# Optimization experiments

Hardware: AMD Instinct MI355X
Metric: run time of the kernel (lower is better)

The kernel has to match this reference:

```python
import jax, jax.numpy as jnp
import numpy as np

B, NH, T, D = 2, 16, 2048, 64

def setup_inputs() -> dict:
    key = jax.random.key(0)
    kq, kk, kv = jax.random.split(key, 3)
    Q = jax.random.normal(kq, (B, NH, T, D), dtype=jnp.float32)
    K = jax.random.normal(kk, (B, NH, T, D), dtype=jnp.float32)
    V = jax.random.normal(kv, (B, NH, T, D), dtype=jnp.float32)
    return {"Q": Q, "K": K, "V": V}

def reference(Q, K, V):
    # scores: [B, nh, T, T]
    Dh = Q.shape[-1]
    scale = 1.0 / jnp.sqrt(jnp.asarray(Dh, Q.dtype))
    scores = jnp.einsum('bhtd,bhsd->bhts', Q, K) * scale
    Tq = Q.shape[2]
    causal = jnp.tril(jnp.ones((Tq, Tq), dtype=bool))
    scores = jnp.where(causal, scores, jnp.asarray(-jnp.inf, scores.dtype))
    attn = jax.nn.softmax(scores, axis=-1)
    return jnp.einsum('bhts,bhsd->bhtd', attn, V)
```

## Files before the change

### kernel.cpp

```cpp
#include <hip/hip_runtime.h>
#include <hip/hip_bf16.h>


typedef __bf16 bf16;
typedef __bf16 bf16x2 __attribute__((ext_vector_type(2)));
typedef __bf16 bf16x4 __attribute__((ext_vector_type(4)));
typedef __bf16 bf16x8 __attribute__((ext_vector_type(8)));
typedef float floatx4 __attribute__((ext_vector_type(4)));

#define T_SEQ 2048
#define DH 64
#define TKS 32
#define BHN 32
#define CEXP 0.18033688011112042f

__device__ __forceinline__ void gload16(const bf16* g, bf16* l) {
    __builtin_amdgcn_global_load_lds(
        (const __attribute__((address_space(1))) void*)g,
        (__attribute__((address_space(3))) void*)l, 16, 0, 0);
}

__global__ __launch_bounds__(256) void prep(const float* __restrict__ K,
                                            const float* __restrict__ V,
                                            bf16* __restrict__ Kb,
                                            bf16* __restrict__ Vt) {
    const int bid = (int)blockIdx.x;
    const int tid = (int)threadIdx.x;
    if (bid < 512) {
        size_t i = ((size_t)bid * 256 + tid) * 8;
        #pragma unroll
        for (int it = 0; it < 4; ++it) {
            float4 a = *(const float4*)(K + i + 0);
            float4 b = *(const float4*)(K + i + 4);
            bf16x8 o;
            o[0]=(bf16)(a.x*CEXP); o[1]=(bf16)(a.y*CEXP); o[2]=(bf16)(a.z*CEXP); o[3]=(bf16)(a.w*CEXP);
            o[4]=(bf16)(b.x*CEXP); o[5]=(bf16)(b.y*CEXP); o[6]=(bf16)(b.z*CEXP); o[7]=(bf16)(b.w*CEXP);
            *(bf16x8*)(Kb + i) = o;
            i += (size_t)512 * 256 * 8;
        }
        return;
    }
    __shared__ bf16 tile[2][64][72];
    const int vb = bid - 512;
    const int bh = vb & (BHN - 1);
    const int tp = (vb >> 5) * 128;
    #pragma unroll
    for (int tt = 0; tt < 2; ++tt) {
        const int r = tid >> 2;
        const int c = (tid & 3) * 16;
        const float* s = V + ((size_t)bh * T_SEQ + tp + tt * 64 + r) * DH + c;
        float4 f0 = *(const float4*)(s + 0);
        float4 f1 = *(const float4*)(s + 4);
        float4 f2 = *(const float4*)(s + 8);
        float4 f3 = *(const float4*)(s + 12);
        bf16x8 p0, p1;
        p0[0]=(bf16)f0.x; p0[1]=(bf16)f0.y; p0[2]=(bf16)f0.z; p0[3]=(bf16)f0.w;
        p0[4]=(bf16)f1.x; p0[5]=(bf16)f1.y; p0[6]=(bf16)f1.z; p0[7]=(bf16)f1.w;
        p1[0]=(bf16)f2.x; p1[1]=(bf16)f2.y; p1[2]=(bf16)f2.z; p1[3]=(bf16)f2.w;
        p1[4]=(bf16)f3.x; p1[5]=(bf16)f3.y; p1[6]=(bf16)f3.z; p1[7]=(bf16)f3.w;
        *(bf16x8*)&tile[tt][r][c + 0] = p0;
        *(bf16x8*)&tile[tt][r][c + 8] = p1;
    }
    __syncthreads();
    #pragma unroll
    for (int tt = 0; tt < 2; ++tt) {
        const int d   = tid >> 2;
        const int tch = (tid & 3) * 16;
        bf16x8 o0, o1;
        #pragma unroll
        for (int j = 0; j < 8; ++j) { o0[j] = tile[tt][tch + j][d]; o1[j] = tile[tt][tch + 8 + j][d]; }
        bf16* o = Vt + ((size_t)bh * DH + d) * T_SEQ + tp + tt * 64 + tch;
        *(bf16x8*)(o + 0) = o0;
        *(bf16x8*)(o + 8) = o1;
    }
}

__global__ __launch_bounds__(256, 2)
void fa_fwd(const float* __restrict__ Qg, const bf16* __restrict__ Kb,
            const bf16* __restrict__ Vt, float* __restrict__ Og)
{
    __shared__ __align__(16) bf16 smem[24576];

    const int gid = (int)blockIdx.x;
    const int bh  = gid & (BHN - 1);
    const int m   = gid >> 5;
    const int B   = 64 - 2 * m;
    const int qh  = (31 - m) * 64;
    const int ql  = m * 64;

    const int tid  = (int)threadIdx.x;
    const int wave = tid >> 6;
    const int lane = tid & 63;
    const int quad = lane >> 4;
    const int l16  = lane & 15;
    const int psw  = (l16 >> 1) & 3;

    const int tw0 = (wave < 2) ? wave * 17 : 34 + (wave - 2) * 16;
    const int tw1 = tw0 + ((wave < 2) ? 17 : 16);

    bf16* W = smem + wave * 6144;

    const bf16* Kbh = Kb + (size_t)bh * (T_SEQ * DH);
    const bf16* Vbh = Vt + (size_t)bh * (DH * T_SEQ);
    const size_t qrb = (size_t)bh * T_SEQ;

    const int rl  = lane >> 3;
    const int kch = (lane & 7) ^ (rl & 7);
    const int vr  = lane >> 2;
    const int vch = (lane & 3) ^ ((lane >> 3) & 3);

    bool heavyNow = (tw0 < B);
    int  qbase    = heavyNow ? qh : ql;
    bool hasPark  = false;

    bf16x8 qb[4][2];
    auto loadQ = [&](int qb0) {
        #pragma unroll
        for (int nt = 0; nt < 4; ++nt) {
            const int qrow = qb0 + nt * 16 + l16;
            #pragma unroll
            for (int kk = 0; kk < 2; ++kk) {
                const float* s = Qg + (qrb + qrow) * DH + kk * 32 + quad * 8;
                float4 f0 = *(const float4*)(s);
                float4 f1 = *(const float4*)(s + 4);
                bf16x8 t;
                t[0]=(bf16)f0.x; t[1]=(bf16)f0.y; t[2]=(bf16)f0.z; t[3]=(bf16)f0.w;
                t[4]=(bf16)f1.x; t[5]=(bf16)f1.y; t[6]=(bf16)f1.z; t[7]=(bf16)f1.w;
                qb[nt][kk] = t;
            }
        }
    };
    loadQ(qbase);

    floatx4 oacc[4][4];
    #pragma unroll
    for (int mt = 0; mt < 4; ++mt)
        #pragma unroll
        for (int nt = 0; nt < 4; ++nt) oacc[mt][nt] = (floatx4){0.f,0.f,0.f,0.f};
    float lpart[4] = {0.f, 0.f, 0.f, 0.f};
    bf16x4 parked[16];
    #pragma unroll
    for (int f = 0; f < 16; ++f) parked[f] = (bf16x4){(bf16)0.f,(bf16)0.f,(bf16)0.f,(bf16)0.f};
    float lpark[4] = {0.f, 0.f, 0.f, 0.f};

    auto kTileOf = [&](int t) { return (t < B) ? t : (t - B); };

    auto stageK = [&](int kt, bf16* dst) {
        const bf16* kg = Kbh + (size_t)kt * TKS * DH;
        #pragma unroll
        for (int g = 0; g < 4; ++g)
            gload16(kg + (size_t)(g * 8 + rl) * DH + kch * 8, dst + g * 512);
    };
    auto stageV = [&](int kt, bf16* dst) {
        const bf16* vg = Vbh + kt * TKS;
        #pragma unroll
        for (int g = 0; g < 4; ++g)
            gload16(vg + (size_t)(g * 16 + vr) * T_SEQ + vch * 8, dst + g * 512);
    };

    auto pk2 = [&](float a, float b) -> unsigned {
        bf16x2 h; h[0] = (bf16)a; h[1] = (bf16)b;
        return __builtin_bit_cast(unsigned, h);
    };

    stageK(kTileOf(tw0), W);
    stageV(kTileOf(tw0), W + 4096);

    for (int t = tw0; t < tw1; ++t) {
        if (heavyNow && t == B) {
            #pragma unroll
            for (int f = 0; f < 16; ++f) {
                bf16x4 w;
                #pragma unroll
                for (int e = 0; e < 4; ++e) w[e] = (bf16)oacc[f >> 2][f & 3][e];
                parked[f] = w;
            }
            #pragma unroll
            for (int nt = 0; nt < 4; ++nt) { lpark[nt] = lpart[nt]; lpart[nt] = 0.f; }
            #pragma unroll
            for (int mt = 0; mt < 4; ++mt)
                #pragma unroll
                for (int nt = 0; nt < 4; ++nt) oacc[mt][nt] = (floatx4){0.f,0.f,0.f,0.f};
            hasPark = true;
            heavyNow = false;
            qbase = ql;
            loadQ(ql);
        }

        const int cur = (t - tw0) & 1;
        bf16* Kcur = W + cur * 2048;
        bf16* Vcur = W + 4096;
        const int kt = kTileOf(t);
        const int k0 = kt * TKS;

        const bool pf = (t + 1 < tw1);
        if (pf) {
            stageK(kTileOf(t + 1), W + (cur ^ 1) * 2048);
            __builtin_amdgcn_s_waitcnt(0x0F78);
        } else {
            __builtin_amdgcn_s_waitcnt(0x0F70);
        }

        floatx4 sa[2][4];
        #pragma unroll
        for (int mt = 0; mt < 2; ++mt)
            #pragma unroll
            for (int nt = 0; nt < 4; ++nt) sa[mt][nt] = (floatx4){0.f,0.f,0.f,0.f};
        __builtin_amdgcn_s_setprio(1);
        #pragma unroll
        for (int kk = 0; kk < 2; ++kk) {
            #pragma unroll
            for (int mt = 0; mt < 2; ++mt) {
                bf16x8 kf = *(const bf16x8*)&Kcur[(mt * 16 + l16) * 64 + (((kk * 4 + quad) ^ (l16 & 7)) * 8)];
                #pragma unroll
                for (int nt = 0; nt < 4; ++nt)
                    sa[mt][nt] = __builtin_amdgcn_mfma_f32_16x16x32_bf16(kf, qb[nt][kk], sa[mt][nt], 0, 0, 0);
            }
        }
        __builtin_amdgcn_s_setprio(0);
        if (k0 + TKS - 1 > qbase) {
            #pragma unroll
            for (int mt = 0; mt < 2; ++mt)
                #pragma unroll
                for (int nt = 0; nt < 4; ++nt) {
                    const int qg = qbase + nt * 16 + l16;
                    #pragma unroll
                    for (int r = 0; r < 4; ++r) {
                        const int keyg = k0 + mt * 16 + quad * 4 + r;
                        if (keyg > qg) sa[mt][nt][r] = -INFINITY;
                    }
                }
        }
        bf16x8 pfr[4];
        #pragma unroll
        for (int nt = 0; nt < 4; ++nt) {
            float p0[4], p1[4];
            #pragma unroll
            for (int r = 0; r < 4; ++r) {
                p0[r] = __builtin_amdgcn_exp2f(sa[0][nt][r]);
                p1[r] = __builtin_amdgcn_exp2f(sa[1][nt][r]);
                lpart[nt] += p0[r] + p1[r];
            }
            unsigned X0 = pk2(p0[0], p0[1]);
            unsigned X1 = pk2(p0[2], p0[3]);
            unsigned Y0 = pk2(p1[0], p1[1]);
            unsigned Y1 = pk2(p1[2], p1[3]);
            asm("v_permlane32_swap_b32 %0, %1" : "+v"(X0), "+v"(Y0));
            asm("v_permlane16_swap_b32 %0, %1" : "+v"(X0), "+v"(Y0));
            asm("v_permlane32_swap_b32 %0, %1" : "+v"(X1), "+v"(Y1));
            asm("v_permlane16_swap_b32 %0, %1" : "+v"(X1), "+v"(Y1));
            uint4 u; u.x = X0; u.y = X1; u.z = Y0; u.w = Y1;
            pfr[nt] = __builtin_bit_cast(bf16x8, u);
        }
        if (pf) __builtin_amdgcn_s_waitcnt(0x0F74);
        bf16x8 vf[4];
        #pragma unroll
        for (int mt = 0; mt < 4; ++mt)
            vf[mt] = *(const bf16x8*)&Vcur[(mt * 16 + l16) * 32 + ((quad ^ psw) * 8)];
        if (pf) {
            __builtin_amdgcn_s_waitcnt(0xC07F);
            stageV(kTileOf(t + 1), Vcur);
        }
        __builtin_amdgcn_s_setprio(1);
        #pragma unroll
        for (int mt = 0; mt < 4; ++mt) {
            #pragma unroll
            for (int nt = 0; nt < 4; ++nt)
                oacc[mt][nt] = __builtin_amdgcn_mfma_f32_16x16x32_bf16(vf[mt], pfr[nt], oacc[mt][nt], 0, 0, 0);
        }
        __builtin_amdgcn_s_setprio(0);
    }

    __syncthreads();
    const bool hH = (tw0 < B);
    const bool hL = (tw1 > B);
    if (wave >= 1 && hH) {
        bf16* a = smem + (wave - 1) * 4608;
        float* al = (float*)(a + 4096);
        #pragma unroll
        for (int f = 0; f < 16; ++f) {
            bf16x4 w;
            if (hasPark) w = parked[f];
            else {
                #pragma unroll
                for (int e = 0; e < 4; ++e) w[e] = (bf16)oacc[f >> 2][f & 3][e];
            }
            *(bf16x4*)&a[(f * 64 + lane) * 4] = w;
        }
        #pragma unroll
        for (int nt = 0; nt < 4; ++nt)
            al[nt * 64 + lane] = hasPark ? lpark[nt] : lpart[nt];
    }
    if (wave >= 2 && hL) {
        bf16* a = smem + (wave + 1) * 4608;
        float* al = (float*)(a + 4096);
        #pragma unroll
        for (int f = 0; f < 16; ++f) {
            bf16x4 w;
            #pragma unroll
            for (int e = 0; e < 4; ++e) w[e] = (bf16)oacc[f >> 2][f & 3][e];
            *(bf16x4*)&a[(f * 64 + lane) * 4] = w;
        }
        #pragma unroll
        for (int nt = 0; nt < 4; ++nt)
            al[nt * 64 + lane] = lpart[nt];
    }
    __syncthreads();

    if (wave <= 1) {
        int qfin;
        if (wave == 0) {
            qfin = qh;
            const int nA = (B > 50) ? 3 : ((B > 34) ? 2 : 1);
            for (int i = 0; i < nA; ++i) {
                const bf16* a = smem + i * 4608;
                const float* al = (const float*)(a + 4096);
                #pragma unroll
                for (int f = 0; f < 16; ++f) {
                    bf16x4 w = *(const bf16x4*)&a[(f * 64 + lane) * 4];
                    #pragma unroll
                    for (int e = 0; e < 4; ++e) oacc[f >> 2][f & 3][e] += (float)w[e];
                }
                #pragma unroll
                for (int nt = 0; nt < 4; ++nt) lpart[nt] += al[nt * 64 + lane];
            }
        } else {
            qfin = ql;
            #pragma unroll
            for (int mt = 0; mt < 4; ++mt)
                #pragma unroll
                for (int nt = 0; nt < 4; ++nt) oacc[mt][nt] = (floatx4){0.f,0.f,0.f,0.f};
            #pragma unroll
            for (int nt = 0; nt < 4; ++nt) lpart[nt] = 0.f;
            const int i0 = (B < 50) ? 3 : 4;
            for (int i = i0; i <= 4; ++i) {
                const bf16* a = smem + i * 4608;
                const float* al = (const float*)(a + 4096);
                #pragma unroll
                for (int f = 0; f < 16; ++f) {
                    bf16x4 w = *(const bf16x4*)&a[(f * 64 + lane) * 4];
                    #pragma unroll
                    for (int e = 0; e < 4; ++e) oacc[f >> 2][f & 3][e] += (float)w[e];
                }
                #pragma unroll
                for (int nt = 0; nt < 4; ++nt) lpart[nt] += al[nt * 64 + lane];
            }
        }
        float invl[4];
        #pragma unroll
        for (int nt = 0; nt < 4; ++nt) {
            float v = lpart[nt];
            v += __shfl_xor(v, 16);
            v += __shfl_xor(v, 32);
            invl[nt] = 1.0f / v;
        }
        #pragma unroll
        for (int nt = 0; nt < 4; ++nt) {
            const size_t qrow = qrb + qfin + nt * 16 + l16;
            #pragma unroll
            for (int mt = 0; mt < 4; ++mt) {
                float4 o;
                o.x = oacc[mt][nt][0] * invl[nt];
                o.y = oacc[mt][nt][1] * invl[nt];
                o.z = oacc[mt][nt][2] * invl[nt];
                o.w = oacc[mt][nt][3] * invl[nt];
                *(float4*)&Og[qrow * DH + mt * 16 + quad * 4] = o;
            }
        }
    }
}

extern "C" void kernel_launch(void* const* d_in, const int* in_sizes, int n_in,
                              void* d_out, int out_size, void* d_ws, size_t ws_size,
                              hipStream_t stream) {
    const float* Q = (const float*)d_in[0];
    const float* K = (const float*)d_in[1];
    const float* V = (const float*)d_in[2];
    float* O = (float*)d_out;
    (void)in_sizes; (void)n_in; (void)out_size; (void)ws_size;

    const size_t nelem = (size_t)BHN * T_SEQ * DH;
    bf16* Kbf = (bf16*)d_ws;
    bf16* Vtb = Kbf + nelem;

    prep<<<dim3(1024), dim3(256), 0, stream>>>(K, V, Kbf, Vtb);
    fa_fwd<<<dim3(512), dim3(256), 0, stream>>>(Q, Kbf, Vtb, O);
}
```

Measured before the change: 120.0 us.

## Replace paired heavy/light query-block balancing with one query block per workgroup

Drops the scheme that paired a heavy and a light 64-row query block in each workgroup (with parked partial accumulators). Each workgroup now handles one query block, and its causal key tiles are split evenly across the four waves. The grid doubles to 1024 blocks, and launch bounds rise to three blocks per CU to improve occupancy and simplify control flow. In exchange, per-block work becomes uneven, so the heavy-first ordering matters for tail balance. The final reduction now splits output rows between two waves.

```diff
diff --git a/kernel.cpp b/kernel.cpp
--- a/kernel.cpp
+++ b/kernel.cpp
@@ -75,18 +75,17 @@
     }
 }
 
-__global__ __launch_bounds__(256, 2)
+__global__ __launch_bounds__(256, 3)
 void fa_fwd(const float* __restrict__ Qg, const bf16* __restrict__ Kb,
             const bf16* __restrict__ Vt, float* __restrict__ Og)
 {
     __shared__ __align__(16) bf16 smem[24576];
 
-    const int gid = (int)blockIdx.x;
-    const int bh  = gid & (BHN - 1);
-    const int m   = gid >> 5;
-    const int B   = 64 - 2 * m;
-    const int qh  = (31 - m) * 64;
-    const int ql  = m * 64;
+    const int gid   = (int)blockIdx.x;
+    const int jt    = 31 - (gid >> 5);
+    const int bh    = gid & (BHN - 1);
+    const int qbase = jt * 64;
+    const int ntile = 2 * jt + 2;
 
     const int tid  = (int)threadIdx.x;
     const int wave = tid >> 6;
@@ -95,8 +94,11 @@
     const int l16  = lane & 15;
     const int psw  = (l16 >> 1) & 3;
 
-    const int tw0 = (wave < 2) ? wave * 17 : 34 + (wave - 2) * 16;
-    const int tw1 = tw0 + ((wave < 2) ? 17 : 16);
+    const int base = ntile >> 2;
+    const int rem  = ntile & 3;
+    const int tw0  = wave * base + ((wave < rem) ? wave : rem);
+    const int cnt  = base + ((wave < rem) ? 1 : 0);
+    const int tw1  = tw0 + cnt;
 
     bf16* W = smem + wave * 6144;
 
@@ -109,15 +111,36 @@
     const int vr  = lane >> 2;
     const int vch = (lane & 3) ^ ((lane >> 3) & 3);
 
-    bool heavyNow = (tw0 < B);
-    int  qbase    = heavyNow ? qh : ql;
-    bool hasPark  = false;
-
-    bf16x8 qb[4][2];
-    auto loadQ = [&](int qb0) {
+    floatx4 oacc[4][4];
+    #pragma unroll
+    for (int mt = 0; mt < 4; ++mt)
+        #pragma unroll
+        for (int nt = 0; nt < 4; ++nt) oacc[mt][nt] = (floatx4){0.f,0.f,0.f,0.f};
+    float lpart[4] = {0.f, 0.f, 0.f, 0.f};
+
+    auto stageK = [&](int kt, bf16* dst) {
+        const bf16* kg = Kbh + (size_t)kt * TKS * DH;
+        #pragma unroll
+        for (int g = 0; g < 4; ++g)
+            gload16(kg + (size_t)(g * 8 + rl) * DH + kch * 8, dst + g * 512);
+    };
+    auto stageV = [&](int kt, bf16* dst) {
+        const bf16* vg = Vbh + kt * TKS;
+        #pragma unroll
+        for (int g = 0; g < 4; ++g)
+            gload16(vg + (size_t)(g * 16 + vr) * T_SEQ + vch * 8, dst + g * 512);
+    };
+
+    auto pk2 = [&](float a, float b) -> unsigned {
+        bf16x2 h; h[0] = (bf16)a; h[1] = (bf16)b;
+        return __builtin_bit_cast(unsigned, h);
+    };
+
+    if (cnt > 0) {
+        bf16x8 qb[4][2];
         #pragma unroll
         for (int nt = 0; nt < 4; ++nt) {
-            const int qrow = qb0 + nt * 16 + l16;
+            const int qrow = qbase + nt * 16 + l16;
             #pragma unroll
             for (int kk = 0; kk < 2; ++kk) {
                 const float* s = Qg + (qrb + qrow) * DH + kk * 32 + quad * 8;
@@ -129,174 +152,102 @@
                 qb[nt][kk] = t;
             }
         }
-    };
-    loadQ(qbase);
-
-    floatx4 oacc[4][4];
-    #pragma unroll
-    for (int mt = 0; mt < 4; ++mt)
-        #pragma unroll
-        for (int nt = 0; nt < 4; ++nt) oacc[mt][nt] = (floatx4){0.f,0.f,0.f,0.f};
-    float lpart[4] = {0.f, 0.f, 0.f, 0.f};
-    bf16x4 parked[16];
-    #pragma unroll
-    for (int f = 0; f < 16; ++f) parked[f] = (bf16x4){(bf16)0.f,(bf16)0.f,(bf16)0.f,(bf16)0.f};
-    float lpark[4] = {0.f, 0.f, 0.f, 0.f};
-
-    auto kTileOf = [&](int t) { return (t < B) ? t : (t - B); };
-
-    auto stageK = [&](int kt, bf16* dst) {
-        const bf16* kg = Kbh + (size_t)kt * TKS * DH;
-        #pragma unroll
-        for (int g = 0; g < 4; ++g)
-            gload16(kg + (size_t)(g * 8 + rl) * DH + kch * 8, dst + g * 512);
-    };
-    auto stageV = [&](int kt, bf16* dst) {
-        const bf16* vg = Vbh + kt * TKS;
-        #pragma unroll
-        for (int g = 0; g < 4; ++g)
-            gload16(vg + (size_t)(g * 16 + vr) * T_SEQ + vch * 8, dst + g * 512);
-    };
-
-    auto pk2 = [&](float a, float b) -> unsigned {
-        bf16x2 h; h[0] = (bf16)a; h[1] = (bf16)b;
-        return __builtin_bit_cast(unsigned, h);
-    };
-
-    stageK(kTileOf(tw0), W);
-    stageV(kTileOf(tw0), W + 4096);
-
-    for (int t = tw0; t < tw1; ++t) {
-        if (heavyNow && t == B) {
-            #pragma unroll
-            for (int f = 0; f < 16; ++f) {
-                bf16x4 w;
-                #pragma unroll
-                for (int e = 0; e < 4; ++e) w[e] = (bf16)oacc[f >> 2][f & 3][e];
-                parked[f] = w;
-            }
-            #pragma unroll
-            for (int nt = 0; nt < 4; ++nt) { lpark[nt] = lpart[nt]; lpart[nt] = 0.f; }
+
+        stageK(tw0, W);
+        stageV(tw0, W + 4096);
+
+        for (int t = tw0; t < tw1; ++t) {
+            const int cur = (t - tw0) & 1;
+            bf16* Kcur = W + cur * 2048;
+            bf16* Vcur = W + 4096;
+            const int k0 = t * TKS;
+
+            const bool pf = (t + 1 < tw1);
+            if (pf) {
+                stageK(t + 1, W + (cur ^ 1) * 2048);
+                __builtin_amdgcn_s_waitcnt(0x0F78);
+            } else {
+                __builtin_amdgcn_s_waitcnt(0x0F70);
+            }
+
+            floatx4 sa[2][4];
+            #pragma unroll
+            for (int mt = 0; mt < 2; ++mt)
+                #pragma unroll
+                for (int nt = 0; nt < 4; ++nt) sa[mt][nt] = (floatx4){0.f,0.f,0.f,0.f};
+            __builtin_amdgcn_s_setprio(1);
+            #pragma unroll
+            for (int kk = 0; kk < 2; ++kk) {
+                #pragma unroll
+                for (int mt = 0; mt < 2; ++mt) {
+                    bf16x8 kf = *(const bf16x8*)&Kcur[(mt * 16 + l16) * 64 + (((kk * 4 + quad) ^ (l16 & 7)) * 8)];
+                    #pragma unroll
+                    for (int nt = 0; nt < 4; ++nt)
+                        sa[mt][nt] = __builtin_amdgcn_mfma_f32_16x16x32_bf16(kf, qb[nt][kk], sa[mt][nt], 0, 0, 0);
+                }
+            }
+            __builtin_amdgcn_s_setprio(0);
+            if (k0 + TKS - 1 > qbase) {
+                #pragma unroll
+                for (int mt = 0; mt < 2; ++mt)
+                    #pragma unroll
+                    for (int nt = 0; nt < 4; ++nt) {
+                        const int qg = qbase + nt * 16 + l16;
+                        #pragma unroll
+                        for (int r = 0; r < 4; ++r) {
+                            const int keyg = k0 + mt * 16 + quad * 4 + r;
+                            if (keyg > qg) sa[mt][nt][r] = -INFINITY;
+                        }
+                    }
+            }
+            bf16x8 pfr[4];
+            #pragma unroll
+            for (int nt = 0; nt < 4; ++nt) {
+                float p0[4], p1[4];
+                #pragma unroll
+                for (int r = 0; r < 4; ++r) {
+                    p0[r] = __builtin_amdgcn_exp2f(sa[0][nt][r]);
+                    p1[r] = __builtin_amdgcn_exp2f(sa[1][nt][r]);
+                    lpart[nt] += p0[r] + p1[r];
+                }
+                unsigned X0 = pk2(p0[0], p0[1]);
+                unsigned X1 = pk2(p0[2], p0[3]);
+                unsigned Y0 = pk2(p1[0], p1[1]);
+                unsigned Y1 = pk2(p1[2], p1[3]);
+                asm("v_permlane32_swap_b32 %0, %1" : "+v"(X0), "+v"(Y0));
+                asm("v_permlane16_swap_b32 %0, %1" : "+v"(X0), "+v"(Y0));
+                asm("v_permlane32_swap_b32 %0, %1" : "+v"(X1), "+v"(Y1));
+                asm("v_permlane16_swap_b32 %0, %1" : "+v"(X1), "+v"(Y1));
+                uint4 u; u.x = X0; u.y = X1; u.z = Y0; u.w = Y1;
+                pfr[nt] = __builtin_bit_cast(bf16x8, u);
+            }
+            if (pf) __builtin_amdgcn_s_waitcnt(0x0F74);
+            bf16x8 vf[4];
             #pragma unroll
             for (int mt = 0; mt < 4; ++mt)
-                #pragma unroll
-                for (int nt = 0; nt < 4; ++nt) oacc[mt][nt] = (floatx4){0.f,0.f,0.f,0.f};
-            hasPark = true;
-            heavyNow = false;
-            qbase = ql;
-            loadQ(ql);
-        }
-
-        const int cur = (t - tw0) & 1;
-        bf16* Kcur = W + cur * 2048;
-        bf16* Vcur = W + 4096;
-        const int kt = kTileOf(t);
-        const int k0 = kt * TKS;
-
-        const bool pf = (t + 1 < tw1);
-        if (pf) {
-            stageK(kTileOf(t + 1), W + (cur ^ 1) * 2048);
-            __builtin_amdgcn_s_waitcnt(0x0F78);
-        } else {
-            __builtin_amdgcn_s_waitcnt(0x0F70);
-        }
-
-        floatx4 sa[2][4];
-        #pragma unroll
-        for (int mt = 0; mt < 2; ++mt)
-            #pragma unroll
-            for (int nt = 0; nt < 4; ++nt) sa[mt][nt] = (floatx4){0.f,0.f,0.f,0.f};
-        __builtin_amdgcn_s_setprio(1);
-        #pragma unroll
-        for (int kk = 0; kk < 2; ++kk) {
-            #pragma unroll
-            for (int mt = 0; mt < 2; ++mt) {
-                bf16x8 kf = *(const bf16x8*)&Kcur[(mt * 16 + l16) * 64 + (((kk * 4 + quad) ^ (l16 & 7)) * 8)];
+                vf[mt] = *(const bf16x8*)&Vcur[(mt * 16 + l16) * 32 + ((quad ^ psw) * 8)];
+            if (pf) {
+                __builtin_amdgcn_s_waitcnt(0xC07F);
+                stageV(t + 1, Vcur);
+            }
+            __builtin_amdgcn_s_setprio(1);
+            #pragma unroll
+            for (int mt = 0; mt < 4; ++mt) {
                 #pragma unroll
                 for (int nt = 0; nt < 4; ++nt)
-                    sa[mt][nt] = __builtin_amdgcn_mfma_f32_16x16x32_bf16(kf, qb[nt][kk], sa[mt][nt], 0, 0, 0);
-            }
-        }
-        __builtin_amdgcn_s_setprio(0);
-        if (k0 + TKS - 1 > qbase) {
-            #pragma unroll
-            for (int mt = 0; mt < 2; ++mt)
-                #pragma unroll
-                for (int nt = 0; nt < 4; ++nt) {
-                    const int qg = qbase + nt * 16 + l16;
-                    #pragma unroll
-                    for (int r = 0; r < 4; ++r) {
-                        const int keyg = k0 + mt * 16 + quad * 4 + r;
-                        if (keyg > qg) sa[mt][nt][r] = -INFINITY;
-                    }
-                }
-        }
-        bf16x8 pfr[4];
-        #pragma unroll
-        for (int nt = 0; nt < 4; ++nt) {
-            float p0[4], p1[4];
-            #pragma unroll
-            for (int r = 0; r < 4; ++r) {
-                p0[r] = __builtin_amdgcn_exp2f(sa[0][nt][r]);
-                p1[r] = __builtin_amdgcn_exp2f(sa[1][nt][r]);
-                lpart[nt] += p0[r] + p1[r];
-            }
-            unsigned X0 = pk2(p0[0], p0[1]);
-            unsigned X1 = pk2(p0[2], p0[3]);
-            unsigned Y0 = pk2(p1[0], p1[1]);
-            unsigned Y1 = pk2(p1[2], p1[3]);
-            asm("v_permlane32_swap_b32 %0, %1" : "+v"(X0), "+v"(Y0));
-            asm("v_permlane16_swap_b32 %0, %1" : "+v"(X0), "+v"(Y0));
-            asm("v_permlane32_swap_b32 %0, %1" : "+v"(X1), "+v"(Y1));
-            asm("v_permlane16_swap_b32 %0, %1" : "+v"(X1), "+v"(Y1));
-            uint4 u; u.x = X0; u.y = X1; u.z = Y0; u.w = Y1;
-            pfr[nt] = __builtin_bit_cast(bf16x8, u);
-        }
-        if (pf) __builtin_amdgcn_s_waitcnt(0x0F74);
-        bf16x8 vf[4];
-        #pragma unroll
-        for (int mt = 0; mt < 4; ++mt)
-            vf[mt] = *(const bf16x8*)&Vcur[(mt * 16 + l16) * 32 + ((quad ^ psw) * 8)];
-        if (pf) {
-            __builtin_amdgcn_s_waitcnt(0xC07F);
-            stageV(kTileOf(t + 1), Vcur);
-        }
-        __builtin_amdgcn_s_setprio(1);
-        #pragma unroll
-        for (int mt = 0; mt < 4; ++mt) {
-            #pragma unroll
-            for (int nt = 0; nt < 4; ++nt)
-                oacc[mt][nt] = __builtin_amdgcn_mfma_f32_16x16x32_bf16(vf[mt], pfr[nt], oacc[mt][nt], 0, 0, 0);
-        }
-        __builtin_amdgcn_s_setprio(0);
+                    oacc[mt][nt] = __builtin_amdgcn_mfma_f32_16x16x32_bf16(vf[mt], pfr[nt], oacc[mt][nt], 0, 0, 0);
+            }
+            __builtin_amdgcn_s_setprio(0);
+        }
     }
 
     __syncthreads();
-    const bool hH = (tw0 < B);
-    const bool hL = (tw1 > B);
-    if (wave >= 1 && hH) {
-        bf16* a = smem + (wave - 1) * 4608;
+    {
+        bf16* a = smem + wave * 4608;
         float* al = (float*)(a + 4096);
         #pragma unroll
         for (int f = 0; f < 16; ++f) {
             bf16x4 w;
-            if (hasPark) w = parked[f];
-            else {
-                #pragma unroll
-                for (int e = 0; e < 4; ++e) w[e] = (bf16)oacc[f >> 2][f & 3][e];
-            }
-            *(bf16x4*)&a[(f * 64 + lane) * 4] = w;
-        }
-        #pragma unroll
-        for (int nt = 0; nt < 4; ++nt)
-            al[nt * 64 + lane] = hasPark ? lpark[nt] : lpart[nt];
-    }
-    if (wave >= 2 && hL) {
-        bf16* a = smem + (wave + 1) * 4608;
-        float* al = (float*)(a + 4096);
-        #pragma unroll
-        for (int f = 0; f < 16; ++f) {
-            bf16x4 w;
             #pragma unroll
             for (int e = 0; e < 4; ++e) w[e] = (bf16)oacc[f >> 2][f & 3][e];
             *(bf16x4*)&a[(f * 64 + lane) * 4] = w;
@@ -308,62 +259,44 @@
     __syncthreads();
 
     if (wave <= 1) {
-        int qfin;
-        if (wave == 0) {
-            qfin = qh;
-            const int nA = (B > 50) ? 3 : ((B > 34) ? 2 : 1);
-            for (int i = 0; i < nA; ++i) {
-                const bf16* a = smem + i * 4608;
-                const float* al = (const float*)(a + 4096);
-                #pragma unroll
-                for (int f = 0; f < 16; ++f) {
-                    bf16x4 w = *(const bf16x4*)&a[(f * 64 + lane) * 4];
-                    #pragma unroll
-                    for (int e = 0; e < 4; ++e) oacc[f >> 2][f & 3][e] += (float)w[e];
-                }
-                #pragma unroll
-                for (int nt = 0; nt < 4; ++nt) lpart[nt] += al[nt * 64 + lane];
-            }
-        } else {
-            qfin = ql;
-            #pragma unroll
-            for (int mt = 0; mt < 4; ++mt)
-                #pragma unroll
-                for (int nt = 0; nt < 4; ++nt) oacc[mt][nt] = (floatx4){0.f,0.f,0.f,0.f};
-            #pragma unroll
-            for (int nt = 0; nt < 4; ++nt) lpart[nt] = 0.f;
-            const int i0 = (B < 50) ? 3 : 4;
-            for (int i = i0; i <= 4; ++i) {
-                const bf16* a = smem + i * 4608;
-                const float* al = (const float*)(a + 4096);
-                #pragma unroll
-                for (int f = 0; f < 16; ++f) {
-                    bf16x4 w = *(const bf16x4*)&a[(f * 64 + lane) * 4];
-                    #pragma unroll
-                    for (int e = 0; e < 4; ++e) oacc[f >> 2][f & 3][e] += (float)w[e];
-                }
-                #pragma unroll
-                for (int nt = 0; nt < 4; ++nt) lpart[nt] += al[nt * 64 + lane];
-            }
-        }
-        float invl[4];
-        #pragma unroll
-        for (int nt = 0; nt < 4; ++nt) {
-            float v = lpart[nt];
+        #pragma unroll
+        for (int mt = 0; mt < 4; ++mt)
+            #pragma unroll
+            for (int nt = 0; nt < 4; ++nt) oacc[mt][nt] = (floatx4){0.f,0.f,0.f,0.f};
+        #pragma unroll
+        for (int nt = 0; nt < 4; ++nt) lpart[nt] = 0.f;
+        for (int i = 0; i < 4; ++i) {
+            const bf16* a = smem + i * 4608;
+            const float* al = (const float*)(a + 4096);
+            #pragma unroll
+            for (int f = 0; f < 16; ++f) {
+                bf16x4 w = *(const bf16x4*)&a[(f * 64 + lane) * 4];
+                #pragma unroll
+                for (int e = 0; e < 4; ++e) oacc[f >> 2][f & 3][e] += (float)w[e];
+            }
+            #pragma unroll
+            for (int nt = 0; nt < 4; ++nt) lpart[nt] += al[nt * 64 + lane];
+        }
+        const int nt0 = wave * 2;
+        float invl[2];
+        #pragma unroll
+        for (int k = 0; k < 2; ++k) {
+            float v = lpart[nt0 + k];
             v += __shfl_xor(v, 16);
             v += __shfl_xor(v, 32);
-            invl[nt] = 1.0f / v;
-        }
-        #pragma unroll
-        for (int nt = 0; nt < 4; ++nt) {
-            const size_t qrow = qrb + qfin + nt * 16 + l16;
+            invl[k] = 1.0f / v;
+        }
+        #pragma unroll
+        for (int k = 0; k < 2; ++k) {
+            const int nt = nt0 + k;
+            const size_t qrow = qrb + qbase + nt * 16 + l16;
             #pragma unroll
             for (int mt = 0; mt < 4; ++mt) {
                 float4 o;
-                o.x = oacc[mt][nt][0] * invl[nt];
-                o.y = oacc[mt][nt][1] * invl[nt];
-                o.z = oacc[mt][nt][2] * invl[nt];
-                o.w = oacc[mt][nt][3] * invl[nt];
+                o.x = oacc[mt][nt][0] * invl[k];
+                o.y = oacc[mt][nt][1] * invl[k];
+                o.z = oacc[mt][nt][2] * invl[k];
+                o.w = oacc[mt][nt][3] * invl[k];
                 *(float4*)&Og[qrow * DH + mt * 16 + quad * 4] = o;
             }
         }
@@ -384,5 +317,5 @@
     bf16* Vtb = Kbf + nelem;
 
     prep<<<dim3(1024), dim3(256), 0, stream>>>(K, V, Kbf, Vtb);
-    fa_fwd<<<dim3(512), dim3(256), 0, stream>>>(Q, Kbf, Vtb, O);
+    fa_fwd<<<dim3(1024), dim3(256), 0, stream>>>(Q, Kbf, Vtb, O);
 }
```

New measurement: 183.6 us. +52.9%, slower.

## Load V fragments directly from global and compute softmax denominator via MFMA

Applied to the files above, without the earlier changes.

V tiles are no longer staged through LDS with async global-to-LDS loads. Each lane now reads its bf16x8 V fragment straight from the transposed V in global memory at the top of each iteration, and the waitcnt sequencing is adjusted to match. The per-row softmax denominator is no longer built from scalar adds plus cross-lane shuffles; it comes from an extra MFMA that multiplies the probability fragments by an all-ones vector. This frees LDS and removes VALU and shuffle work, at the cost of four extra MFMAs per tile, uncached global reads exposed inside the loop, and bf16 rounding of the probabilities in the denominator sum.

```diff
diff --git a/kernel.cpp b/kernel.cpp
--- a/kernel.cpp
+++ b/kernel.cpp
@@ -93,7 +93,6 @@
     const int lane = tid & 63;
     const int quad = lane >> 4;
     const int l16  = lane & 15;
-    const int psw  = (l16 >> 1) & 3;
 
     const int tw0 = (wave < 2) ? wave * 17 : 34 + (wave - 2) * 16;
     const int tw1 = tw0 + ((wave < 2) ? 17 : 16);
@@ -106,8 +105,7 @@
 
     const int rl  = lane >> 3;
     const int kch = (lane & 7) ^ (rl & 7);
-    const int vr  = lane >> 2;
-    const int vch = (lane & 3) ^ ((lane >> 3) & 3);
+    const bf16* Vrow = Vbh + (size_t)l16 * T_SEQ + quad * 8;
 
     bool heavyNow = (tw0 < B);
     int  qbase    = heavyNow ? qh : ql;
@@ -137,12 +135,18 @@
     for (int mt = 0; mt < 4; ++mt)
         #pragma unroll
         for (int nt = 0; nt < 4; ++nt) oacc[mt][nt] = (floatx4){0.f,0.f,0.f,0.f};
-    float lpart[4] = {0.f, 0.f, 0.f, 0.f};
+    floatx4 dacc[4];
+    #pragma unroll
+    for (int nt = 0; nt < 4; ++nt) dacc[nt] = (floatx4){0.f,0.f,0.f,0.f};
     bf16x4 parked[16];
     #pragma unroll
     for (int f = 0; f < 16; ++f) parked[f] = (bf16x4){(bf16)0.f,(bf16)0.f,(bf16)0.f,(bf16)0.f};
     float lpark[4] = {0.f, 0.f, 0.f, 0.f};
 
+    bf16x8 onef;
+    #pragma unroll
+    for (int j = 0; j < 8; ++j) onef[j] = (bf16)1.0f;
+
     auto kTileOf = [&](int t) { return (t < B) ? t : (t - B); };
 
     auto stageK = [&](int kt, bf16* dst) {
@@ -150,12 +154,6 @@
         #pragma unroll
         for (int g = 0; g < 4; ++g)
             gload16(kg + (size_t)(g * 8 + rl) * DH + kch * 8, dst + g * 512);
-    };
-    auto stageV = [&](int kt, bf16* dst) {
-        const bf16* vg = Vbh + kt * TKS;
-        #pragma unroll
-        for (int g = 0; g < 4; ++g)
-            gload16(vg + (size_t)(g * 16 + vr) * T_SEQ + vch * 8, dst + g * 512);
     };
 
     auto pk2 = [&](float a, float b) -> unsigned {
@@ -164,7 +162,6 @@
     };
 
     stageK(kTileOf(tw0), W);
-    stageV(kTileOf(tw0), W + 4096);
 
     for (int t = tw0; t < tw1; ++t) {
         if (heavyNow && t == B) {
@@ -176,7 +173,7 @@
                 parked[f] = w;
             }
             #pragma unroll
-            for (int nt = 0; nt < 4; ++nt) { lpark[nt] = lpart[nt]; lpart[nt] = 0.f; }
+            for (int nt = 0; nt < 4; ++nt) { lpark[nt] = dacc[nt][0]; dacc[nt] = (floatx4){0.f,0.f,0.f,0.f}; }
             #pragma unroll
             for (int mt = 0; mt < 4; ++mt)
                 #pragma unroll
@@ -189,16 +186,20 @@
 
         const int cur = (t - tw0) & 1;
         bf16* Kcur = W + cur * 2048;
-        bf16* Vcur = W + 4096;
         const int kt = kTileOf(t);
         const int k0 = kt * TKS;
+
+        bf16x8 vf[4];
+        #pragma unroll
+        for (int mt = 0; mt < 4; ++mt)
+            vf[mt] = *(const bf16x8*)(Vrow + (size_t)(mt * 16) * T_SEQ + k0);
 
         const bool pf = (t + 1 < tw1);
         if (pf) {
             stageK(kTileOf(t + 1), W + (cur ^ 1) * 2048);
             __builtin_amdgcn_s_waitcnt(0x0F78);
         } else {
-            __builtin_amdgcn_s_waitcnt(0x0F70);
+            __builtin_amdgcn_s_waitcnt(0x0F74);
         }
 
         floatx4 sa[2][4];
@@ -239,7 +240,6 @@
             for (int r = 0; r < 4; ++r) {
                 p0[r] = __builtin_amdgcn_exp2f(sa[0][nt][r]);
                 p1[r] = __builtin_amdgcn_exp2f(sa[1][nt][r]);
-                lpart[nt] += p0[r] + p1[r];
             }
             unsigned X0 = pk2(p0[0], p0[1]);
             unsigned X1 = pk2(p0[2], p0[3]);
@@ -253,14 +253,7 @@
             pfr[nt] = __builtin_bit_cast(bf16x8, u);
         }
         if (pf) __builtin_amdgcn_s_waitcnt(0x0F74);
-        bf16x8 vf[4];
-        #pragma unroll
-        for (int mt = 0; mt < 4; ++mt)
-            vf[mt] = *(const bf16x8*)&Vcur[(mt * 16 + l16) * 32 + ((quad ^ psw) * 8)];
-        if (pf) {
-            __builtin_amdgcn_s_waitcnt(0xC07F);
-            stageV(kTileOf(t + 1), Vcur);
-        }
+        else    __builtin_amdgcn_s_waitcnt(0x0F70);
         __builtin_amdgcn_s_setprio(1);
         #pragma unroll
         for (int mt = 0; mt < 4; ++mt) {
@@ -268,6 +261,9 @@
             for (int nt = 0; nt < 4; ++nt)
                 oacc[mt][nt] = __builtin_amdgcn_mfma_f32_16x16x32_bf16(vf[mt], pfr[nt], oacc[mt][nt], 0, 0, 0);
         }
+        #pragma unroll
+        for (int nt = 0; nt < 4; ++nt)
+            dacc[nt] = __builtin_amdgcn_mfma_f32_16x16x32_bf16(onef, pfr[nt], dacc[nt], 0, 0, 0);
         __builtin_amdgcn_s_setprio(0);
     }
 
@@ -289,7 +285,7 @@
         }
         #pragma unroll
         for (int nt = 0; nt < 4; ++nt)
-            al[nt * 64 + lane] = hasPark ? lpark[nt] : lpart[nt];
+            al[nt * 64 + lane] = hasPark ? lpark[nt] : dacc[nt][0];
     }
     if (wave >= 2 && hL) {
         bf16* a = smem + (wave + 1) * 4608;
@@ -303,14 +299,17 @@
         }
         #pragma unroll
         for (int nt = 0; nt < 4; ++nt)
-            al[nt * 64 + lane] = lpart[nt];
+            al[nt * 64 + lane] = dacc[nt][0];
     }
     __syncthreads();
 
     if (wave <= 1) {
         int qfin;
+        float lden[4];
         if (wave == 0) {
             qfin = qh;
+            #pragma unroll
+            for (int nt = 0; nt < 4; ++nt) lden[nt] = dacc[nt][0];
             const int nA = (B > 50) ? 3 : ((B > 34) ? 2 : 1);
             for (int i = 0; i < nA; ++i) {
                 const bf16* a = smem + i * 4608;
@@ -322,7 +321,7 @@
                     for (int e = 0; e < 4; ++e) oacc[f >> 2][f & 3][e] += (float)w[e];
                 }
                 #pragma unroll
-                for (int nt = 0; nt < 4; ++nt) lpart[nt] += al[nt * 64 + lane];
+                for (int nt = 0; nt < 4; ++nt) lden[nt] += al[nt * 64 + lane];
             }
         } else {
             qfin = ql;
@@ -331,7 +330,7 @@
                 #pragma unroll
                 for (int nt = 0; nt < 4; ++nt) oacc[mt][nt] = (floatx4){0.f,0.f,0.f,0.f};
             #pragma unroll
-            for (int nt = 0; nt < 4; ++nt) lpart[nt] = 0.f;
+            for (int nt = 0; nt < 4; ++nt) lden[nt] = 0.f;
             const int i0 = (B < 50) ? 3 : 4;
             for (int i = i0; i <= 4; ++i) {
                 const bf16* a = smem + i * 4608;
@@ -343,27 +342,20 @@
                     for (int e = 0; e < 4; ++e) oacc[f >> 2][f & 3][e] += (float)w[e];
                 }
                 #pragma unroll
-                for (int nt = 0; nt < 4; ++nt) lpart[nt] += al[nt * 64 + lane];
-            }
-        }
-        float invl[4];
+                for (int nt = 0; nt < 4; ++nt) lden[nt] += al[nt * 64 + lane];
+            }
+        }
         #pragma unroll
         for (int nt = 0; nt < 4; ++nt) {
-            float v = lpart[nt];
-            v += __shfl_xor(v, 16);
-            v += __shfl_xor(v, 32);
-            invl[nt] = 1.0f / v;
-        }
-        #pragma unroll
-        for (int nt = 0; nt < 4; ++nt) {
+            const float invl = 1.0f / lden[nt];
             const size_t qrow = qrb + qfin + nt * 16 + l16;
             #pragma unroll
             for (int mt = 0; mt < 4; ++mt) {
                 float4 o;
-                o.x = oacc[mt][nt][0] * invl[nt];
-                o.y = oacc[mt][nt][1] * invl[nt];
-                o.z = oacc[mt][nt][2] * invl[nt];
-                o.w = oacc[mt][nt][3] * invl[nt];
+                o.x = oacc[mt][nt][0] * invl;
+                o.y = oacc[mt][nt][1] * invl;
+                o.z = oacc[mt][nt][2] * invl;
+                o.w = oacc[mt][nt][3] * invl;
                 *(float4*)&Og[qrow * DH + mt * 16 + quad * 4] = o;
             }
         }
```

Result: no change. 121.9 us (+1.6%).
